# Kernel tuning notes

Hardware: AMD Instinct MI355X
Metric: run time of the kernel (lower is better)

## Reference

```python
import jax, jax.numpy as jnp
import numpy as np

B, L, D, H = 2, 4096, 512, 8
HD = D // H  # head_dim = 64


def setup_inputs() -> dict:
    key = jax.random.key(0)
    ks = jax.random.split(key, 5)
    s = 0.02
    return {
        "x": jax.random.normal(ks[0], (B, L, D), dtype=jnp.float32),
        "w_qkv": jax.random.normal(ks[1], (D, 3 * D), dtype=jnp.float32) * s,
        "b_qkv": jax.random.normal(ks[2], (3 * D,), dtype=jnp.float32) * s,
        "w_o": jax.random.normal(ks[3], (D, D), dtype=jnp.float32) * s,
        "b_o": jax.random.normal(ks[4], (D,), dtype=jnp.float32) * s,
    }


def reference(x, w_qkv, b_qkv, w_o, b_o):
    b, l, _ = x.shape
    # QKV projection, then split heads: [B, L, 3D] -> [B, H, L, 3*HD]
    qkv = x @ w_qkv + b_qkv
    qkv = qkv.reshape(b, l, H, 3 * HD).transpose(0, 2, 1, 3)
    q, k, v = jnp.split(qkv, 3, axis=-1)  # each [B, H, L, HD]
    scale = 1.0 / jnp.sqrt(jnp.asarray(HD, dtype=q.dtype))
    # full score matrix [B, H, L, L], softmax in float32 (matches .float() cast)
    scores = jnp.einsum('bhld,bhsd->bhls', q, k) * scale
    attn = jax.nn.softmax(scores.astype(jnp.float32), axis=-1).astype(q.dtype)
    values = jnp.einsum('bhls,bhsd->bhld', attn, v)  # [B, H, L, HD]
    values = values.transpose(0, 2, 1, 3).reshape(b, l, D)
    return values @ w_o + b_o
```

## Files before the change

### kernel.cpp

```cpp
#include <hip/hip_runtime.h>


#define B_  2
#define L_  4096
#define D_  512
#define H_  8
#define HD_ 64
#define BH_ (B_*H_)
#define M_  (B_*L_)
#define QKVN (3*D_)
#define HEADSZ (BH_*L_*HD_)

typedef unsigned short ushort;
typedef unsigned int uint;
typedef __bf16 bf16x8 __attribute__((ext_vector_type(8)));
typedef float  f32x4  __attribute__((ext_vector_type(4)));

typedef const __attribute__((address_space(1))) void g_void;
typedef __attribute__((address_space(3))) void l_void;

__device__ __forceinline__ ushort f2bf(float f) {
    __bf16 h = (__bf16)f;
    return __builtin_bit_cast(ushort, h);
}

__global__ __launch_bounds__(256)
void prep_k(const float* __restrict__ x, ushort* __restrict__ xb,
            const float* __restrict__ wq, ushort* __restrict__ wtq,
            const float* __restrict__ wo, ushort* __restrict__ wto)
{
    int bid = blockIdx.x, tid = threadIdx.x;
    if (bid < 4096) {
        int idx = bid * 256 + tid;
        float4 v = ((const float4*)x)[idx];
        ushort4 o; o.x = f2bf(v.x); o.y = f2bf(v.y); o.z = f2bf(v.z); o.w = f2bf(v.w);
        ((ushort4*)xb)[idx] = o;
    } else if (bid < 7168) {
        int idx = (bid - 4096) * 256 + tid;
        int c = idx / D_, r = idx % D_;
        wtq[idx] = f2bf(wq[r * QKVN + c]);
    } else {
        int idx = (bid - 7168) * 256 + tid;
        int c = idx / D_, r = idx % D_;
        wto[idx] = f2bf(wo[r * D_ + c]);
    }
}

#define TP 66
__global__ __launch_bounds__(256)
void transpose_v(const ushort* __restrict__ V, ushort* __restrict__ VT) {
    __shared__ ushort T[64 * TP];
    const int tid = threadIdx.x;
    const int bh = blockIdx.y;
    const int l0 = blockIdx.x * 64;
    const int base = bh * (L_ * HD_);
    #pragma unroll
    for (int i = 0; i < 2; i++) {
        int c = i * 256 + tid;
        int l = c >> 3, dc = (c & 7) * 8;
        uint4 v = *(const uint4*)&V[base + (l0 + l) * HD_ + dc];
        uint* p = (uint*)&T[l * TP + dc];
        p[0] = v.x; p[1] = v.y; p[2] = v.z; p[3] = v.w;
    }
    __syncthreads();
    #pragma unroll
    for (int p = 0; p < 2; p++) {
        int c = p * 256 + tid;
        int d = c >> 3, lb = c & 7;
        ushort tmp[8];
        #pragma unroll
        for (int j = 0; j < 8; j++) tmp[j] = T[(lb * 8 + j) * TP + d];
        *(uint4*)&VT[base + d * L_ + l0 + lb * 8] = *(uint4*)tmp;
    }
}

__global__ __launch_bounds__(256)
void gemm_bt(const ushort* __restrict__ A, const ushort* __restrict__ Bt,
             const float* __restrict__ bias, void* __restrict__ out,
             int M, int N, int K, int mode)
{
    __shared__ ushort As[128 * 32];
    __shared__ ushort Bs[128 * 32];

    const int tid  = threadIdx.x;
    const int lane = tid & 63;
    const int wid  = tid >> 6;
    const int wm   = wid >> 1, wn = wid & 1;
    const int lr   = lane & 15;
    const int quad = lane >> 4;
    const int tm = blockIdx.x, tn = blockIdx.y;

    f32x4 acc[4][4] = {};
    const int arow = tm * 128;
    const int brow = tn * 128;

    for (int k0 = 0; k0 < K; k0 += 32) {
        #pragma unroll
        for (int i = 0; i < 2; i++) {
            int c   = i * 256 + tid;
            int row = c >> 2;
            int kk  = (c & 3) * 8;
            __builtin_amdgcn_global_load_lds(
                (g_void*)&A[(size_t)(arow + row) * K + k0 + kk],
                (l_void*)&As[c * 8], 16, 0, 0);
            __builtin_amdgcn_global_load_lds(
                (g_void*)&Bt[(size_t)(brow + row) * K + k0 + kk],
                (l_void*)&Bs[c * 8], 16, 0, 0);
        }
        __syncthreads();

        bf16x8 af[4], bfr[4];
        #pragma unroll
        for (int t = 0; t < 4; t++) {
            af [t] = *(const bf16x8*)&As[(wm * 64 + t * 16 + lr) * 32 + quad * 8];
            bfr[t] = *(const bf16x8*)&Bs[(wn * 64 + t * 16 + lr) * 32 + quad * 8];
        }
        #pragma unroll
        for (int mt = 0; mt < 4; mt++)
            #pragma unroll
            for (int nt = 0; nt < 4; nt++)
                acc[mt][nt] = __builtin_amdgcn_mfma_f32_16x16x32_bf16(
                    af[mt], bfr[nt], acc[mt][nt], 0, 0, 0);
        __syncthreads();
    }

    #pragma unroll
    for (int nt = 0; nt < 4; nt++) {
        int col = tn * 128 + wn * 64 + nt * 16 + lr;
        float bv = bias[col];
        #pragma unroll
        for (int mt = 0; mt < 4; mt++) {
            #pragma unroll
            for (int r = 0; r < 4; r++) {
                int row = tm * 128 + wm * 64 + mt * 16 + quad * 4 + r;
                float v = acc[mt][nt][r] + bv;
                if (mode == 0) {
                    ((float*)out)[(size_t)row * N + col] = v;
                } else {
                    int d = col & 63;
                    int g = col >> 6;
                    int which = g % 3;
                    int h = g / 3;
                    int b = row >> 12;
                    int l = row & (L_ - 1);
                    ((ushort*)out)[which * HEADSZ + (((b * H_ + h) * L_ + l) * HD_) + d]
                        = f2bf(v);
                }
            }
        }
    }
}

#define SP 72
__global__ __launch_bounds__(512)
void attn_k(const ushort* __restrict__ Q, const ushort* __restrict__ K,
            const ushort* __restrict__ VT, ushort* __restrict__ O)
{
    __shared__ ushort Ks[2][64 * SP];
    __shared__ ushort Vt[2][64 * SP];
    __shared__ ushort Pw[8][16 * SP];

    const int tid  = threadIdx.x;
    const int lane = tid & 63;
    const int wid  = tid >> 6;
    const int lr   = lane & 15;
    const int quad = lane >> 4;
    const int bh = blockIdx.y;
    const int q0 = blockIdx.x * 128;
    const int base = bh * (L_ * HD_);

    const int rrS = tid >> 3;
    const int ccS = (tid & 7) * 8;

    const int qrow = q0 + wid * 16 + lr;
    const bf16x8 qf0 = *(const bf16x8*)&Q[base + qrow * HD_ +      quad * 8];
    const bf16x8 qf1 = *(const bf16x8*)&Q[base + qrow * HD_ + 32 + quad * 8];

    float l_part[4] = {0.f, 0.f, 0.f, 0.f};
    f32x4 o_acc[4] = {};
    const float C2 = 0.18033688011112042f;

    {
        uint4 a = *(const uint4*)&K [base + rrS * HD_ + ccS];
        uint4 b = *(const uint4*)&VT[base + rrS * L_  + ccS];
        *(uint4*)&Ks[0][rrS * SP + ccS] = a;
        *(uint4*)&Vt[0][rrS * SP + ccS] = b;
    }

    for (int t = 0; t < L_ / 64; t++) {
        const int cur = t & 1;
        __syncthreads();

        uint4 na, nb;
        const bool pf = (t + 1) < (L_ / 64);
        if (pf) {
            int s1 = (t + 1) * 64;
            na = *(const uint4*)&K [base + (s1 + rrS) * HD_ + ccS];
            nb = *(const uint4*)&VT[base + rrS * L_ + s1 + ccS];
        }

        f32x4 sc[4] = {};
        #pragma unroll
        for (int nt = 0; nt < 4; nt++) {
            bf16x8 b0 = *(const bf16x8*)&Ks[cur][(nt * 16 + lr) * SP +      quad * 8];
            bf16x8 b1 = *(const bf16x8*)&Ks[cur][(nt * 16 + lr) * SP + 32 + quad * 8];
            sc[nt] = __builtin_amdgcn_mfma_f32_16x16x32_bf16(qf0, b0, sc[nt], 0, 0, 0);
            sc[nt] = __builtin_amdgcn_mfma_f32_16x16x32_bf16(qf1, b1, sc[nt], 0, 0, 0);
        }

        #pragma unroll
        for (int nt = 0; nt < 4; nt++) {
            #pragma unroll
            for (int r = 0; r < 4; r++) {
                float p = exp2f(sc[nt][r] * C2);
                l_part[r] += p;
                Pw[wid][(quad * 4 + r) * SP + nt * 16 + lr] = f2bf(p);
            }
        }

        #pragma unroll
        for (int ks = 0; ks < 2; ks++) {
            bf16x8 pa = *(const bf16x8*)&Pw[wid][lr * SP + ks * 32 + quad * 8];
            #pragma unroll
            for (int nt = 0; nt < 4; nt++) {
                bf16x8 vb = *(const bf16x8*)&Vt[cur][(nt * 16 + lr) * SP + ks * 32 + quad * 8];
                o_acc[nt] = __builtin_amdgcn_mfma_f32_16x16x32_bf16(pa, vb, o_acc[nt], 0, 0, 0);
            }
        }

        if (pf) {
            *(uint4*)&Ks[cur ^ 1][rrS * SP + ccS] = na;
            *(uint4*)&Vt[cur ^ 1][rrS * SP + ccS] = nb;
        }
    }

    #pragma unroll
    for (int off = 8; off >= 1; off >>= 1)
        #pragma unroll
        for (int r = 0; r < 4; r++)
            l_part[r] += __shfl_xor(l_part[r], off, 64);

    float inv[4];
    #pragma unroll
    for (int r = 0; r < 4; r++) inv[r] = 1.0f / l_part[r];

    const int b = bh >> 3, h = bh & 7;
    #pragma unroll
    for (int nt = 0; nt < 4; nt++) {
        #pragma unroll
        for (int r = 0; r < 4; r++) {
            int row = q0 + wid * 16 + quad * 4 + r;
            int d   = nt * 16 + lr;
            O[((b * L_ + row) * D_) + h * HD_ + d] = f2bf(o_acc[nt][r] * inv[r]);
        }
    }
}

extern "C" void kernel_launch(void* const* d_in, const int* in_sizes, int n_in,
                              void* d_out, int out_size, void* d_ws, size_t ws_size,
                              hipStream_t stream)
{
    const float* x     = (const float*)d_in[0];
    const float* w_qkv = (const float*)d_in[1];
    const float* b_qkv = (const float*)d_in[2];
    const float* w_o   = (const float*)d_in[3];
    const float* b_o   = (const float*)d_in[4];

    char* ws = (char*)d_ws;
    size_t o = 0;
    ushort* xb   = (ushort*)(ws + o); o += (size_t)M_ * D_ * 2;
    ushort* qkv  = (ushort*)(ws + o); o += (size_t)3 * HEADSZ * 2;
    ushort* attn = (ushort*)(ws + o); o += (size_t)M_ * D_ * 2;
    ushort* wtq  = (ushort*)(ws + o); o += (size_t)QKVN * D_ * 2;
    ushort* wto  = (ushort*)(ws + o);
    ushort* vt   = xb;

    hipLaunchKernelGGL(prep_k, dim3(8192), dim3(256), 0, stream,
                       x, xb, w_qkv, wtq, w_o, wto);
    hipLaunchKernelGGL(gemm_bt, dim3(M_ / 128, QKVN / 128), dim3(256), 0, stream,
                       xb, wtq, b_qkv, (void*)qkv, M_, QKVN, D_, 1);
    hipLaunchKernelGGL(transpose_v, dim3(L_ / 64, BH_), dim3(256), 0, stream,
                       qkv + 2 * HEADSZ, vt);
    hipLaunchKernelGGL(attn_k, dim3(L_ / 128, BH_), dim3(512), 0, stream,
                       qkv, qkv + HEADSZ, vt, attn);
    hipLaunchKernelGGL(gemm_bt, dim3(M_ / 128, D_ / 128), dim3(256), 0, stream,
                       attn, wto, b_o, d_out, M_, D_, D_, 0);
}
```

Baseline: 253.0 us.

## Rewrite attention kernel with 32x32 MFMA, register-resident P, and direct LDS loads

The attention kernel switches from 16x16x32 to 32x32x16 MFMA and computes S^T = K·Q so that P stays in registers. P is repacked with v_permlane32_swap instead of a round trip through shared memory. K/V tiles are loaded with global_load_lds into XOR-swizzled unpadded LDS, and each block now covers 256 query rows with the grid remapped so each XCD handles fixed heads. The softmax scale is folded into Q in the QKV GEMM epilogue, and s_setprio wraps the MFMA phases. The trade-offs are higher register pressure from 16-wide accumulators and reliance on gfx950-specific instructions. Like before, it keeps no running max, so it assumes exponents stay small enough not to overflow.

```diff
diff --git a/kernel.cpp b/kernel.cpp
--- a/kernel.cpp
+++ b/kernel.cpp
@@ -15,13 +15,20 @@
 typedef unsigned int uint;
 typedef __bf16 bf16x8 __attribute__((ext_vector_type(8)));
 typedef float  f32x4  __attribute__((ext_vector_type(4)));
+typedef float  f32x16 __attribute__((ext_vector_type(16)));
 
 typedef const __attribute__((address_space(1))) void g_void;
 typedef __attribute__((address_space(3))) void l_void;
+
+#define C2_ 0.18033688011112042f
 
 __device__ __forceinline__ ushort f2bf(float f) {
     __bf16 h = (__bf16)f;
     return __builtin_bit_cast(ushort, h);
+}
+
+__device__ __forceinline__ uint pack2(float lo, float hi) {
+    return (uint)f2bf(lo) | ((uint)f2bf(hi) << 16);
 }
 
 __global__ __launch_bounds__(256)
@@ -143,6 +150,7 @@
                     int h = g / 3;
                     int b = row >> 12;
                     int l = row & (L_ - 1);
+                    if (which == 0) v *= C2_;
                     ((ushort*)out)[which * HEADSZ + (((b * H_ + h) * L_ + l) * HD_) + d]
                         = f2bf(v);
                 }
@@ -151,108 +159,112 @@
     }
 }
 
-#define SP 72
 __global__ __launch_bounds__(512)
 void attn_k(const ushort* __restrict__ Q, const ushort* __restrict__ K,
             const ushort* __restrict__ VT, ushort* __restrict__ O)
 {
-    __shared__ ushort Ks[2][64 * SP];
-    __shared__ ushort Vt[2][64 * SP];
-    __shared__ ushort Pw[8][16 * SP];
+    __shared__ __align__(16) ushort Ks[2][64 * 64];
+    __shared__ __align__(16) ushort Vt[2][64 * 64];
+    __shared__ float Linv[8][32];
 
     const int tid  = threadIdx.x;
     const int lane = tid & 63;
     const int wid  = tid >> 6;
-    const int lr   = lane & 15;
-    const int quad = lane >> 4;
-    const int bh = blockIdx.y;
-    const int q0 = blockIdx.x * 128;
-    const int base = bh * (L_ * HD_);
-
-    const int rrS = tid >> 3;
-    const int ccS = (tid & 7) * 8;
-
-    const int qrow = q0 + wid * 16 + lr;
-    const bf16x8 qf0 = *(const bf16x8*)&Q[base + qrow * HD_ +      quad * 8];
-    const bf16x8 qf1 = *(const bf16x8*)&Q[base + qrow * HD_ + 32 + quad * 8];
-
-    float l_part[4] = {0.f, 0.f, 0.f, 0.f};
-    f32x4 o_acc[4] = {};
-    const float C2 = 0.18033688011112042f;
-
+    const int l31  = lane & 31;
+    const int hi   = lane >> 5;
+
+    const int wg  = blockIdx.x;
+    const int xcd = wg & 7, sl = wg >> 3;
+    const int bh  = (xcd << 1) | (sl >> 4);
+    const int q0  = (sl & 15) * 256;
+    const size_t base = (size_t)bh * (L_ * HD_);
+
+    const int sr  = tid >> 3;
+    const int scx = ((tid & 7) ^ (sr & 7)) * 8;
+    const ushort* Kg = K  + base + sr * HD_ + scx;
+    const ushort* Vg = VT + base + (size_t)sr * L_ + scx;
+
+    bf16x8 qf[4];
     {
-        uint4 a = *(const uint4*)&K [base + rrS * HD_ + ccS];
-        uint4 b = *(const uint4*)&VT[base + rrS * L_  + ccS];
-        *(uint4*)&Ks[0][rrS * SP + ccS] = a;
-        *(uint4*)&Vt[0][rrS * SP + ccS] = b;
-    }
+        const ushort* qp = Q + base + (size_t)(q0 + wid * 32 + l31) * HD_ + hi * 8;
+        #pragma unroll
+        for (int ks = 0; ks < 4; ks++) qf[ks] = *(const bf16x8*)(qp + ks * 16);
+    }
+
+    const int swz = (l31 & 7) << 4;
+    int cbe[4];
+    #pragma unroll
+    for (int ks = 0; ks < 4; ks++) cbe[ks] = ((ks * 32 + hi * 16) ^ swz) >> 1;
+    const int kr0 = l31 * 64, kr1 = (32 + l31) * 64;
+
+    __builtin_amdgcn_global_load_lds((g_void*)Kg, (l_void*)&Ks[0][tid * 8], 16, 0, 0);
+    __builtin_amdgcn_global_load_lds((g_void*)Vg, (l_void*)&Vt[0][tid * 8], 16, 0, 0);
+
+    f32x16 o0 = {}, o1 = {};
+    float l4[4] = {0.f, 0.f, 0.f, 0.f};
 
     for (int t = 0; t < L_ / 64; t++) {
         const int cur = t & 1;
         __syncthreads();
 
-        uint4 na, nb;
-        const bool pf = (t + 1) < (L_ / 64);
-        if (pf) {
-            int s1 = (t + 1) * 64;
-            na = *(const uint4*)&K [base + (s1 + rrS) * HD_ + ccS];
-            nb = *(const uint4*)&VT[base + rrS * L_ + s1 + ccS];
-        }
-
-        f32x4 sc[4] = {};
-        #pragma unroll
-        for (int nt = 0; nt < 4; nt++) {
-            bf16x8 b0 = *(const bf16x8*)&Ks[cur][(nt * 16 + lr) * SP +      quad * 8];
-            bf16x8 b1 = *(const bf16x8*)&Ks[cur][(nt * 16 + lr) * SP + 32 + quad * 8];
-            sc[nt] = __builtin_amdgcn_mfma_f32_16x16x32_bf16(qf0, b0, sc[nt], 0, 0, 0);
-            sc[nt] = __builtin_amdgcn_mfma_f32_16x16x32_bf16(qf1, b1, sc[nt], 0, 0, 0);
-        }
-
-        #pragma unroll
-        for (int nt = 0; nt < 4; nt++) {
-            #pragma unroll
-            for (int r = 0; r < 4; r++) {
-                float p = exp2f(sc[nt][r] * C2);
-                l_part[r] += p;
-                Pw[wid][(quad * 4 + r) * SP + nt * 16 + lr] = f2bf(p);
-            }
-        }
-
-        #pragma unroll
-        for (int ks = 0; ks < 2; ks++) {
-            bf16x8 pa = *(const bf16x8*)&Pw[wid][lr * SP + ks * 32 + quad * 8];
-            #pragma unroll
-            for (int nt = 0; nt < 4; nt++) {
-                bf16x8 vb = *(const bf16x8*)&Vt[cur][(nt * 16 + lr) * SP + ks * 32 + quad * 8];
-                o_acc[nt] = __builtin_amdgcn_mfma_f32_16x16x32_bf16(pa, vb, o_acc[nt], 0, 0, 0);
-            }
-        }
-
-        if (pf) {
-            *(uint4*)&Ks[cur ^ 1][rrS * SP + ccS] = na;
-            *(uint4*)&Vt[cur ^ 1][rrS * SP + ccS] = nb;
-        }
-    }
-
-    #pragma unroll
-    for (int off = 8; off >= 1; off >>= 1)
-        #pragma unroll
-        for (int r = 0; r < 4; r++)
-            l_part[r] += __shfl_xor(l_part[r], off, 64);
-
-    float inv[4];
-    #pragma unroll
-    for (int r = 0; r < 4; r++) inv[r] = 1.0f / l_part[r];
+        if (t + 1 < L_ / 64) {
+            __builtin_amdgcn_global_load_lds(
+                (g_void*)(Kg + (size_t)(t + 1) * 64 * HD_),
+                (l_void*)&Ks[cur ^ 1][tid * 8], 16, 0, 0);
+            __builtin_amdgcn_global_load_lds(
+                (g_void*)(Vg + (t + 1) * 64),
+                (l_void*)&Vt[cur ^ 1][tid * 8], 16, 0, 0);
+        }
+
+        f32x16 sA = {}, sB = {};
+        __builtin_amdgcn_s_setprio(1);
+        #pragma unroll
+        for (int ks = 0; ks < 4; ks++) {
+            bf16x8 k0 = *(const bf16x8*)&Ks[cur][kr0 + cbe[ks]];
+            bf16x8 k1 = *(const bf16x8*)&Ks[cur][kr1 + cbe[ks]];
+            sA = __builtin_amdgcn_mfma_f32_32x32x16_bf16(k0, qf[ks], sA, 0, 0, 0);
+            sB = __builtin_amdgcn_mfma_f32_32x32x16_bf16(k1, qf[ks], sB, 0, 0, 0);
+        }
+        __builtin_amdgcn_s_setprio(0);
+
+        #pragma unroll
+        for (int i = 0; i < 16; i++) { sA[i] = exp2f(sA[i]); sB[i] = exp2f(sB[i]); }
+        #pragma unroll
+        for (int i = 0; i < 16; i++) l4[i & 3] += sA[i] + sB[i];
+
+        __builtin_amdgcn_s_setprio(1);
+        #pragma unroll
+        for (int ks = 0; ks < 4; ks++) {
+            const f32x16& P = (ks >> 1) ? sB : sA;
+            const int r0 = 8 * (ks & 1);
+            uint a0 = pack2(P[r0 + 0], P[r0 + 1]);
+            uint a1 = pack2(P[r0 + 2], P[r0 + 3]);
+            uint b0 = pack2(P[r0 + 4], P[r0 + 5]);
+            uint b1 = pack2(P[r0 + 6], P[r0 + 7]);
+            asm("v_permlane32_swap_b32 %0, %1" : "+v"(a0), "+v"(b0));
+            asm("v_permlane32_swap_b32 %0, %1" : "+v"(a1), "+v"(b1));
+            uint4 w; w.x = a0; w.y = a1; w.z = b0; w.w = b1;
+            bf16x8 pa = __builtin_bit_cast(bf16x8, w);
+            bf16x8 v0 = *(const bf16x8*)&Vt[cur][kr0 + cbe[ks]];
+            bf16x8 v1 = *(const bf16x8*)&Vt[cur][kr1 + cbe[ks]];
+            o0 = __builtin_amdgcn_mfma_f32_32x32x16_bf16(pa, v0, o0, 0, 0, 0);
+            o1 = __builtin_amdgcn_mfma_f32_32x32x16_bf16(pa, v1, o1, 0, 0, 0);
+        }
+        __builtin_amdgcn_s_setprio(0);
+    }
+
+    float lp = (l4[0] + l4[1]) + (l4[2] + l4[3]);
+    lp += __shfl_xor(lp, 32, 64);
+    if (hi == 0) Linv[wid][l31] = 1.0f / lp;
 
     const int b = bh >> 3, h = bh & 7;
     #pragma unroll
-    for (int nt = 0; nt < 4; nt++) {
-        #pragma unroll
-        for (int r = 0; r < 4; r++) {
-            int row = q0 + wid * 16 + quad * 4 + r;
-            int d   = nt * 16 + lr;
-            O[((b * L_ + row) * D_) + h * HD_ + d] = f2bf(o_acc[nt][r] * inv[r]);
-        }
+    for (int r = 0; r < 16; r++) {
+        const int qrl = (r & 3) + 8 * (r >> 2) + 4 * hi;
+        const float inv = Linv[wid][qrl];
+        const size_t row = (size_t)(b * L_ + q0 + wid * 32 + qrl) * D_ + h * HD_ + l31;
+        O[row]      = f2bf(o0[r] * inv);
+        O[row + 32] = f2bf(o1[r] * inv);
     }
 }
 
@@ -281,7 +293,7 @@
                        xb, wtq, b_qkv, (void*)qkv, M_, QKVN, D_, 1);
     hipLaunchKernelGGL(transpose_v, dim3(L_ / 64, BH_), dim3(256), 0, stream,
                        qkv + 2 * HEADSZ, vt);
-    hipLaunchKernelGGL(attn_k, dim3(L_ / 128, BH_), dim3(512), 0, stream,
+    hipLaunchKernelGGL(attn_k, dim3(256), dim3(512), 0, stream,
                        qkv, qkv + HEADSZ, vt, attn);
     hipLaunchKernelGGL(gemm_bt, dim3(M_ / 128, D_ / 128), dim3(256), 0, stream,
                        attn, wto, b_o, d_out, M_, D_, D_, 0);
```

Result: no change. 251.6 us (-0.6%).
